# Kernel tuning notes

Hardware: AMD Instinct MI355X
Metric: run time of the kernel (lower is better)

Reference implementation:

```python
import jax, jax.numpy as jnp
import numpy as np

N_ITEMS = 100000
N_USERS = 16384
HIST = 50
TEXT_DIM = 256
GCN_DIM = 128
HIDDEN_DIM = 512
TOWER_DIM = 128


def _l2norm(x, eps=1e-12):
    # F.normalize(dim=1): x / max(||x||, eps)
    n = jnp.sqrt(jnp.sum(x * x, axis=1, keepdims=True))
    return x / jnp.maximum(n, eps)


def setup_inputs() -> dict:
    key = jax.random.key(0)
    ks = jax.random.split(key, 10)
    s1i = 1.0 / np.sqrt(TEXT_DIM + GCN_DIM)
    s2i = 1.0 / np.sqrt(HIDDEN_DIM)
    s1u = 1.0 / np.sqrt(GCN_DIM + TOWER_DIM)
    return {
        "item_text_emb": jax.random.normal(ks[0], (N_ITEMS, TEXT_DIM), jnp.float32),
        "gcn_item_emb": jax.random.normal(ks[1], (N_ITEMS, GCN_DIM), jnp.float32),
        "gcn_user_emb": jax.random.normal(ks[2], (N_USERS, GCN_DIM), jnp.float32),
        "hist_idx": jax.random.randint(ks[3], (N_USERS, HIST), 0, N_ITEMS),
        "W1i": jax.random.normal(ks[4], (TEXT_DIM + GCN_DIM, HIDDEN_DIM), jnp.float32) * s1i,
        "b1i": jnp.zeros((HIDDEN_DIM,), jnp.float32),
        "W2i": jax.random.normal(ks[5], (HIDDEN_DIM, TOWER_DIM), jnp.float32) * s2i,
        "b2i": jnp.zeros((TOWER_DIM,), jnp.float32),
        "W1u": jax.random.normal(ks[6], (GCN_DIM + TOWER_DIM, HIDDEN_DIM), jnp.float32) * s1u,
        "b1u": jnp.zeros((HIDDEN_DIM,), jnp.float32),
        "W2u": jax.random.normal(ks[7], (HIDDEN_DIM, TOWER_DIM), jnp.float32) * s2i,
        "b2u": jnp.zeros((TOWER_DIM,), jnp.float32),
    }


def reference(item_text_emb, gcn_item_emb, gcn_user_emb, hist_idx,
              W1i, b1i, W2i, b2i, W1u, b1u, W2u, b2u):
    # encode_items: MLP over concat(text, gcn) features, then L2 normalize
    item_feat = jnp.concatenate([item_text_emb, gcn_item_emb], axis=1)  # [N_items, text+gcn]
    h = jax.nn.relu(item_feat @ W1i + b1i)
    item_emb = _l2norm(h @ W2i + b2i)  # [N_items, TOWER_DIM]
    # encode_users: per-user gather of history item embeddings + mean pooling
    hist = jnp.mean(item_emb[hist_idx], axis=1)  # [N_users, TOWER_DIM]
    fused = jnp.concatenate([gcn_user_emb, hist], axis=1)
    hu = jax.nn.relu(fused @ W1u + b1u)
    user_emb = _l2norm(hu @ W2u + b2u)  # [N_users, TOWER_DIM]
    return user_emb
```

## Files before the change

### kernel.cpp

```cpp
#include <hip/hip_runtime.h>
#include <hip/hip_bf16.h>

#define HIST 50
#define N_ITEMS 100000
#define N_USERS 16384

typedef __bf16 bf8 __attribute__((ext_vector_type(8)));
typedef float  f4  __attribute__((ext_vector_type(4)));

__device__ __forceinline__ unsigned short f2bf(float x) {
    unsigned u = __builtin_bit_cast(unsigned, x);
    u += 0x7fffu + ((u >> 16) & 1u);
    return (unsigned short)(u >> 16);
}
__device__ __forceinline__ float bf2f(unsigned b) {
    unsigned u = b << 16;
    return __builtin_bit_cast(float, u);
}

__global__ void pack_weights(const float* __restrict__ W1i, const float* __restrict__ W2i,
                             const float* __restrict__ W1u, const float* __restrict__ W2u,
                             unsigned short* __restrict__ dstbase)
{
    int i = blockIdx.x * 256 + threadIdx.x;
    const float* W; unsigned short* dst; int N, KS, loc;
    if (i < 24576)      { W = W1i; dst = dstbase;          N = 512; KS = 12; loc = i; }
    else if (i < 32768) { W = W2i; dst = dstbase + 196608; N = 128; KS = 16; loc = i - 24576; }
    else if (i < 49152) { W = W1u; dst = dstbase + 262144; N = 512; KS = 8;  loc = i - 32768; }
    else                { W = W2u; dst = dstbase + 393216; N = 128; KS = 16; loc = i - 49152; }
    int l = loc & 63, fi = loc >> 6;
    int ks = fi % KS, nt = fi / KS;
    int q = l >> 4, c = l & 15;
    const float* src = W + (size_t)(ks * 32 + q * 8) * N + nt * 16 + c;
    unsigned o[4];
    #pragma unroll
    for (int k = 0; k < 4; ++k) {
        unsigned lo = f2bf(src[(2 * k) * N]);
        unsigned hi = f2bf(src[(2 * k + 1) * N]);
        o[k] = lo | (hi << 16);
    }
    uint4 v; v.x = o[0]; v.y = o[1]; v.z = o[2]; v.w = o[3];
    ((uint4*)dst)[(size_t)(nt * KS + ks) * 64 + l] = v;
}

template<int NR, int KS1, int ASTR, bool OUT_BF16>
__device__ __forceinline__ void tower_core(
    unsigned short* U, const float* b1s, const float* b2s, float* sumsq,
    const bf8* __restrict__ w1f, const bf8* __restrict__ w2f,
    void* __restrict__ outp, int row0, int tid)
{
    const int HSTR = 520;
    const int l = tid & 63, w = tid >> 6;
    const int q = l >> 4, c = l & 15;

    f4 acc1[NR][4];
    #pragma unroll
    for (int i = 0; i < NR; ++i)
        #pragma unroll
        for (int j = 0; j < 4; ++j) acc1[i][j] = (f4)0.0f;

    const unsigned short* ap = U + c * ASTR + q * 8;
    bf8 bcur[4], bnxt[4];
    #pragma unroll
    for (int nt = 0; nt < 4; ++nt)
        bcur[nt] = w1f[(size_t)((w * 4 + nt) * KS1 + 0) * 64 + l];
    #pragma unroll
    for (int ks = 0; ks < KS1; ++ks) {
        if (ks + 1 < KS1) {
            #pragma unroll
            for (int nt = 0; nt < 4; ++nt)
                bnxt[nt] = w1f[(size_t)((w * 4 + nt) * KS1 + ks + 1) * 64 + l];
        }
        bf8 a[NR];
        #pragma unroll
        for (int rt = 0; rt < NR; ++rt)
            a[rt] = *(const bf8*)(ap + rt * 16 * ASTR + ks * 32);
        #pragma unroll
        for (int rt = 0; rt < NR; ++rt)
            #pragma unroll
            for (int nt = 0; nt < 4; ++nt)
                acc1[rt][nt] = __builtin_amdgcn_mfma_f32_16x16x32_bf16(a[rt], bcur[nt], acc1[rt][nt], 0, 0, 0);
        #pragma unroll
        for (int nt = 0; nt < 4; ++nt) bcur[nt] = bnxt[nt];
    }
    __syncthreads();

    #pragma unroll
    for (int nt = 0; nt < 4; ++nt) {
        int col = w * 64 + nt * 16 + c;
        float bias = b1s[col];
        #pragma unroll
        for (int rt = 0; rt < NR; ++rt)
            #pragma unroll
            for (int reg = 0; reg < 4; ++reg) {
                float h = fmaxf(acc1[rt][nt][reg] + bias, 0.0f);
                U[(rt * 16 + q * 4 + reg) * HSTR + col] = f2bf(h);
            }
    }
    __syncthreads();

    constexpr int NR2 = NR / 2;
    const int rg = w >> 2, jj = w & 3;
    f4 acc2[NR2][2];
    #pragma unroll
    for (int i = 0; i < NR2; ++i) { acc2[i][0] = (f4)0.0f; acc2[i][1] = (f4)0.0f; }

    const unsigned short* hp = U + (size_t)(rg * NR2 * 16 + c) * HSTR + q * 8;
    bf8 ccur[2], cnxt[2];
    ccur[0] = w2f[(size_t)((jj * 2 + 0) * 16 + 0) * 64 + l];
    ccur[1] = w2f[(size_t)((jj * 2 + 1) * 16 + 0) * 64 + l];
    #pragma unroll
    for (int ks = 0; ks < 16; ++ks) {
        if (ks + 1 < 16) {
            cnxt[0] = w2f[(size_t)((jj * 2 + 0) * 16 + ks + 1) * 64 + l];
            cnxt[1] = w2f[(size_t)((jj * 2 + 1) * 16 + ks + 1) * 64 + l];
        }
        bf8 a[NR2];
        #pragma unroll
        for (int i = 0; i < NR2; ++i)
            a[i] = *(const bf8*)(hp + i * 16 * HSTR + ks * 32);
        #pragma unroll
        for (int i = 0; i < NR2; ++i) {
            acc2[i][0] = __builtin_amdgcn_mfma_f32_16x16x32_bf16(a[i], ccur[0], acc2[i][0], 0, 0, 0);
            acc2[i][1] = __builtin_amdgcn_mfma_f32_16x16x32_bf16(a[i], ccur[1], acc2[i][1], 0, 0, 0);
        }
        ccur[0] = cnxt[0]; ccur[1] = cnxt[1];
    }

    float v[NR2][2][4];
    #pragma unroll
    for (int i = 0; i < NR2; ++i)
        #pragma unroll
        for (int j = 0; j < 2; ++j) {
            float bias = b2s[jj * 32 + j * 16 + c];
            #pragma unroll
            for (int reg = 0; reg < 4; ++reg)
                v[i][j][reg] = acc2[i][j][reg] + bias;
        }
    #pragma unroll
    for (int i = 0; i < NR2; ++i)
        #pragma unroll
        for (int reg = 0; reg < 4; ++reg) {
            float s = v[i][0][reg] * v[i][0][reg] + v[i][1][reg] * v[i][1][reg];
            s += __shfl_xor(s, 1); s += __shfl_xor(s, 2);
            s += __shfl_xor(s, 4); s += __shfl_xor(s, 8);
            if (c == 0) atomicAdd(&sumsq[rg * NR2 * 16 + i * 16 + q * 4 + reg], s);
        }
    __syncthreads();
    #pragma unroll
    for (int i = 0; i < NR2; ++i)
        #pragma unroll
        for (int reg = 0; reg < 4; ++reg) {
            int row = rg * NR2 * 16 + i * 16 + q * 4 + reg;
            float inv = 1.0f / fmaxf(sqrtf(sumsq[row]), 1e-12f);
            #pragma unroll
            for (int j = 0; j < 2; ++j) {
                int col = jj * 32 + j * 16 + c;
                float o = v[i][j][reg] * inv;
                if (OUT_BF16)
                    ((unsigned short*)outp)[(size_t)(row0 + row) * 128 + col] = f2bf(o);
                else
                    ((float*)outp)[(size_t)(row0 + row) * 128 + col] = o;
            }
        }
}

#define ASI 392
#define ASU 264

__global__ __launch_bounds__(512, 4) void item_kernel(
    const float* __restrict__ text, const float* __restrict__ gcn,
    const bf8* __restrict__ w1f, const float* __restrict__ b1,
    const bf8* __restrict__ w2f, const float* __restrict__ b2,
    unsigned short* __restrict__ item_bf)
{
    __shared__ __align__(16) unsigned short U[32 * 520];
    __shared__ float b1s[512], b2s[128], sumsq[32];
    const int tid = threadIdx.x;
    const int row0 = blockIdx.x * 32;
    const float4* t4 = (const float4*)text;
    const float4* g4 = (const float4*)gcn;
    #pragma unroll
    for (int j = 0; j < 4; ++j) {
        int idx = tid + j * 512; int r = idx >> 6, c4 = idx & 63;
        float4 x = t4[(size_t)(row0 + r) * 64 + c4];
        ushort4 s; s.x = f2bf(x.x); s.y = f2bf(x.y); s.z = f2bf(x.z); s.w = f2bf(x.w);
        *(ushort4*)(U + r * ASI + c4 * 4) = s;
    }
    #pragma unroll
    for (int j = 0; j < 2; ++j) {
        int idx = tid + j * 512; int r = idx >> 5, c4 = idx & 31;
        float4 x = g4[(size_t)(row0 + r) * 32 + c4];
        ushort4 s; s.x = f2bf(x.x); s.y = f2bf(x.y); s.z = f2bf(x.z); s.w = f2bf(x.w);
        *(ushort4*)(U + r * ASI + 256 + c4 * 4) = s;
    }
    b1s[tid] = b1[tid];
    if (tid < 128) b2s[tid] = b2[tid];
    if (tid < 32)  sumsq[tid] = 0.0f;
    __syncthreads();
    tower_core<2, 12, ASI, true>(U, b1s, b2s, sumsq, w1f, w2f, item_bf, row0, tid);
}

__global__ __launch_bounds__(512, 4) void user_kernel(
    const float* __restrict__ gcnu, const int* __restrict__ hist,
    const unsigned short* __restrict__ item_bf,
    const bf8* __restrict__ w1f, const float* __restrict__ b1,
    const bf8* __restrict__ w2f, const float* __restrict__ b2,
    float* __restrict__ outp)
{
    __shared__ __align__(16) unsigned short U[32 * 520];
    __shared__ float b1s[512], b2s[128], sumsq[32];
    const int tid = threadIdx.x;
    const int u0 = blockIdx.x * 32;
    int* hist_s = (int*)(U + 32 * ASU);
    const float4* g4 = (const float4*)gcnu;
    #pragma unroll
    for (int j = 0; j < 2; ++j) {
        int idx = tid + j * 512; int r = idx >> 5, c4 = idx & 31;
        float4 x = g4[(size_t)(u0 + r) * 32 + c4];
        ushort4 s; s.x = f2bf(x.x); s.y = f2bf(x.y); s.z = f2bf(x.z); s.w = f2bf(x.w);
        *(ushort4*)(U + r * ASU + c4 * 4) = s;
    }
    for (int k = tid; k < 32 * HIST; k += 512)
        hist_s[k] = hist[(size_t)u0 * HIST + k];
    b1s[tid] = b1[tid];
    if (tid < 128) b2s[tid] = b2[tid];
    if (tid < 32)  sumsq[tid] = 0.0f;
    __syncthreads();
    {
        const int u = tid >> 4, g = tid & 15;
        int ids[HIST];
        #pragma unroll
        for (int t = 0; t < HIST; ++t) ids[t] = hist_s[u * HIST + t];
        float f[8];
        #pragma unroll
        for (int k = 0; k < 8; ++k) f[k] = 0.0f;
        #pragma unroll
        for (int t = 0; t < HIST; ++t) {
            uint4 x = *(const uint4*)(item_bf + (size_t)ids[t] * 128 + g * 8);
            unsigned vs[4] = {x.x, x.y, x.z, x.w};
            #pragma unroll
            for (int k = 0; k < 4; ++k) {
                f[2 * k]     += bf2f(vs[k] & 0xffffu);
                f[2 * k + 1] += bf2f(vs[k] >> 16);
            }
        }
        unsigned o[4];
        #pragma unroll
        for (int k = 0; k < 4; ++k)
            o[k] = (unsigned)f2bf(f[2 * k] * 0.02f) | ((unsigned)f2bf(f[2 * k + 1] * 0.02f) << 16);
        uint4 s; s.x = o[0]; s.y = o[1]; s.z = o[2]; s.w = o[3];
        *(uint4*)(U + u * ASU + 128 + g * 8) = s;
    }
    __syncthreads();
    tower_core<2, 8, ASU, false>(U, b1s, b2s, sumsq, w1f, w2f, outp, u0, tid);
}

extern "C" void kernel_launch(void* const* d_in, const int* in_sizes, int n_in,
                              void* d_out, int out_size, void* d_ws, size_t ws_size,
                              hipStream_t stream) {
    const float* text = (const float*)d_in[0];
    const float* gcni = (const float*)d_in[1];
    const float* gcnu = (const float*)d_in[2];
    const int*   hist = (const int*)d_in[3];
    const float* W1i  = (const float*)d_in[4];
    const float* b1i  = (const float*)d_in[5];
    const float* W2i  = (const float*)d_in[6];
    const float* b2i  = (const float*)d_in[7];
    const float* W1u  = (const float*)d_in[8];
    const float* b1u  = (const float*)d_in[9];
    const float* W2u  = (const float*)d_in[10];
    const float* b2u  = (const float*)d_in[11];
    float* out = (float*)d_out;

    unsigned short* itemb = (unsigned short*)d_ws;
    unsigned short* pw = itemb + 12800000;

    pack_weights<<<224, 256, 0, stream>>>(W1i, W2i, W1u, W2u, pw);
    item_kernel<<<N_ITEMS / 32, 512, 0, stream>>>(
        text, gcni, (const bf8*)pw, b1i, (const bf8*)(pw + 196608), b2i, itemb);
    user_kernel<<<N_USERS / 32, 512, 0, stream>>>(
        gcnu, hist, itemb, (const bf8*)(pw + 262144), b1u, (const bf8*)(pw + 393216), b2u, out);
}
```

Baseline: 305.7 us.

## Halve user-tower block rows and split history gather across two half-waves

The user kernel now processes 16 users per block instead of 32, doubling the grid to 1024 blocks and raising the occupancy hint to 8 blocks per CU. The history gather splits each user's 50 items across two 16-lane groups that are combined with a cross-lane shuffle, and tower_core gains an NR=1 specialization for its second GEMM stage. The aim is more parallelism and memory-level concurrency in the latency-bound gather across the 256 CUs. The cost is that each block reloads the user-tower weights for half as many rows, which doubles that weight traffic, and the MFMA tiles are less fully used.

```diff
diff --git a/kernel.cpp b/kernel.cpp
--- a/kernel.cpp
+++ b/kernel.cpp
@@ -99,70 +99,110 @@
     }
     __syncthreads();
 
-    constexpr int NR2 = NR / 2;
-    const int rg = w >> 2, jj = w & 3;
-    f4 acc2[NR2][2];
-    #pragma unroll
-    for (int i = 0; i < NR2; ++i) { acc2[i][0] = (f4)0.0f; acc2[i][1] = (f4)0.0f; }
-
-    const unsigned short* hp = U + (size_t)(rg * NR2 * 16 + c) * HSTR + q * 8;
-    bf8 ccur[2], cnxt[2];
-    ccur[0] = w2f[(size_t)((jj * 2 + 0) * 16 + 0) * 64 + l];
-    ccur[1] = w2f[(size_t)((jj * 2 + 1) * 16 + 0) * 64 + l];
-    #pragma unroll
-    for (int ks = 0; ks < 16; ++ks) {
-        if (ks + 1 < 16) {
-            cnxt[0] = w2f[(size_t)((jj * 2 + 0) * 16 + ks + 1) * 64 + l];
-            cnxt[1] = w2f[(size_t)((jj * 2 + 1) * 16 + ks + 1) * 64 + l];
-        }
-        bf8 a[NR2];
+    if constexpr (NR >= 2) {
+        constexpr int NR2 = NR / 2;
+        const int rg = w >> 2, jj = w & 3;
+        f4 acc2[NR2][2];
+        #pragma unroll
+        for (int i = 0; i < NR2; ++i) { acc2[i][0] = (f4)0.0f; acc2[i][1] = (f4)0.0f; }
+
+        const unsigned short* hp = U + (size_t)(rg * NR2 * 16 + c) * HSTR + q * 8;
+        bf8 ccur[2], cnxt[2];
+        ccur[0] = w2f[(size_t)((jj * 2 + 0) * 16 + 0) * 64 + l];
+        ccur[1] = w2f[(size_t)((jj * 2 + 1) * 16 + 0) * 64 + l];
+        #pragma unroll
+        for (int ks = 0; ks < 16; ++ks) {
+            if (ks + 1 < 16) {
+                cnxt[0] = w2f[(size_t)((jj * 2 + 0) * 16 + ks + 1) * 64 + l];
+                cnxt[1] = w2f[(size_t)((jj * 2 + 1) * 16 + ks + 1) * 64 + l];
+            }
+            bf8 a[NR2];
+            #pragma unroll
+            for (int i = 0; i < NR2; ++i)
+                a[i] = *(const bf8*)(hp + i * 16 * HSTR + ks * 32);
+            #pragma unroll
+            for (int i = 0; i < NR2; ++i) {
+                acc2[i][0] = __builtin_amdgcn_mfma_f32_16x16x32_bf16(a[i], ccur[0], acc2[i][0], 0, 0, 0);
+                acc2[i][1] = __builtin_amdgcn_mfma_f32_16x16x32_bf16(a[i], ccur[1], acc2[i][1], 0, 0, 0);
+            }
+            ccur[0] = cnxt[0]; ccur[1] = cnxt[1];
+        }
+
+        float v[NR2][2][4];
         #pragma unroll
         for (int i = 0; i < NR2; ++i)
-            a[i] = *(const bf8*)(hp + i * 16 * HSTR + ks * 32);
-        #pragma unroll
-        for (int i = 0; i < NR2; ++i) {
-            acc2[i][0] = __builtin_amdgcn_mfma_f32_16x16x32_bf16(a[i], ccur[0], acc2[i][0], 0, 0, 0);
-            acc2[i][1] = __builtin_amdgcn_mfma_f32_16x16x32_bf16(a[i], ccur[1], acc2[i][1], 0, 0, 0);
-        }
-        ccur[0] = cnxt[0]; ccur[1] = cnxt[1];
-    }
-
-    float v[NR2][2][4];
-    #pragma unroll
-    for (int i = 0; i < NR2; ++i)
-        #pragma unroll
-        for (int j = 0; j < 2; ++j) {
-            float bias = b2s[jj * 32 + j * 16 + c];
-            #pragma unroll
-            for (int reg = 0; reg < 4; ++reg)
-                v[i][j][reg] = acc2[i][j][reg] + bias;
-        }
-    #pragma unroll
-    for (int i = 0; i < NR2; ++i)
+            #pragma unroll
+            for (int j = 0; j < 2; ++j) {
+                float bias = b2s[jj * 32 + j * 16 + c];
+                #pragma unroll
+                for (int reg = 0; reg < 4; ++reg)
+                    v[i][j][reg] = acc2[i][j][reg] + bias;
+            }
+        #pragma unroll
+        for (int i = 0; i < NR2; ++i)
+            #pragma unroll
+            for (int reg = 0; reg < 4; ++reg) {
+                float s = v[i][0][reg] * v[i][0][reg] + v[i][1][reg] * v[i][1][reg];
+                s += __shfl_xor(s, 1); s += __shfl_xor(s, 2);
+                s += __shfl_xor(s, 4); s += __shfl_xor(s, 8);
+                if (c == 0) atomicAdd(&sumsq[rg * NR2 * 16 + i * 16 + q * 4 + reg], s);
+            }
+        __syncthreads();
+        #pragma unroll
+        for (int i = 0; i < NR2; ++i)
+            #pragma unroll
+            for (int reg = 0; reg < 4; ++reg) {
+                int row = rg * NR2 * 16 + i * 16 + q * 4 + reg;
+                float inv = 1.0f / fmaxf(sqrtf(sumsq[row]), 1e-12f);
+                #pragma unroll
+                for (int j = 0; j < 2; ++j) {
+                    int col = jj * 32 + j * 16 + c;
+                    float o = v[i][j][reg] * inv;
+                    if (OUT_BF16)
+                        ((unsigned short*)outp)[(size_t)(row0 + row) * 128 + col] = f2bf(o);
+                    else
+                        ((float*)outp)[(size_t)(row0 + row) * 128 + col] = o;
+                }
+            }
+    } else {
+        const int jj = w;
+        f4 acc2 = (f4)0.0f;
+        const unsigned short* hp = U + (size_t)c * HSTR + q * 8;
+        bf8 ccur = w2f[(size_t)(jj * 16 + 0) * 64 + l];
+        bf8 cnxt = ccur;
+        #pragma unroll
+        for (int ks = 0; ks < 16; ++ks) {
+            if (ks + 1 < 16)
+                cnxt = w2f[(size_t)(jj * 16 + ks + 1) * 64 + l];
+            bf8 a = *(const bf8*)(hp + ks * 32);
+            acc2 = __builtin_amdgcn_mfma_f32_16x16x32_bf16(a, ccur, acc2, 0, 0, 0);
+            ccur = cnxt;
+        }
+
+        float v[4];
+        float bias = b2s[jj * 16 + c];
+        #pragma unroll
+        for (int reg = 0; reg < 4; ++reg) v[reg] = acc2[reg] + bias;
         #pragma unroll
         for (int reg = 0; reg < 4; ++reg) {
-            float s = v[i][0][reg] * v[i][0][reg] + v[i][1][reg] * v[i][1][reg];
+            float s = v[reg] * v[reg];
             s += __shfl_xor(s, 1); s += __shfl_xor(s, 2);
             s += __shfl_xor(s, 4); s += __shfl_xor(s, 8);
-            if (c == 0) atomicAdd(&sumsq[rg * NR2 * 16 + i * 16 + q * 4 + reg], s);
-        }
-    __syncthreads();
-    #pragma unroll
-    for (int i = 0; i < NR2; ++i)
+            if (c == 0) atomicAdd(&sumsq[q * 4 + reg], s);
+        }
+        __syncthreads();
         #pragma unroll
         for (int reg = 0; reg < 4; ++reg) {
-            int row = rg * NR2 * 16 + i * 16 + q * 4 + reg;
+            int row = q * 4 + reg;
             float inv = 1.0f / fmaxf(sqrtf(sumsq[row]), 1e-12f);
-            #pragma unroll
-            for (int j = 0; j < 2; ++j) {
-                int col = jj * 32 + j * 16 + c;
-                float o = v[i][j][reg] * inv;
-                if (OUT_BF16)
-                    ((unsigned short*)outp)[(size_t)(row0 + row) * 128 + col] = f2bf(o);
-                else
-                    ((float*)outp)[(size_t)(row0 + row) * 128 + col] = o;
-            }
-        }
+            int col = jj * 16 + c;
+            float o = v[reg] * inv;
+            if (OUT_BF16)
+                ((unsigned short*)outp)[(size_t)(row0 + row) * 128 + col] = f2bf(o);
+            else
+                ((float*)outp)[(size_t)(row0 + row) * 128 + col] = o;
+        }
+    }
 }
 
 #define ASI 392
@@ -201,43 +241,41 @@
     tower_core<2, 12, ASI, true>(U, b1s, b2s, sumsq, w1f, w2f, item_bf, row0, tid);
 }
 
-__global__ __launch_bounds__(512, 4) void user_kernel(
+__global__ __launch_bounds__(512, 8) void user_kernel(
     const float* __restrict__ gcnu, const int* __restrict__ hist,
     const unsigned short* __restrict__ item_bf,
     const bf8* __restrict__ w1f, const float* __restrict__ b1,
     const bf8* __restrict__ w2f, const float* __restrict__ b2,
     float* __restrict__ outp)
 {
-    __shared__ __align__(16) unsigned short U[32 * 520];
-    __shared__ float b1s[512], b2s[128], sumsq[32];
+    __shared__ __align__(16) unsigned short U[16 * 520];
+    __shared__ float b1s[512], b2s[128], sumsq[16];
     const int tid = threadIdx.x;
-    const int u0 = blockIdx.x * 32;
-    int* hist_s = (int*)(U + 32 * ASU);
+    const int u0 = blockIdx.x * 16;
+    int* hist_s = (int*)(U + 16 * ASU);
     const float4* g4 = (const float4*)gcnu;
-    #pragma unroll
-    for (int j = 0; j < 2; ++j) {
-        int idx = tid + j * 512; int r = idx >> 5, c4 = idx & 31;
+    {
+        int r = tid >> 5, c4 = tid & 31;
         float4 x = g4[(size_t)(u0 + r) * 32 + c4];
         ushort4 s; s.x = f2bf(x.x); s.y = f2bf(x.y); s.z = f2bf(x.z); s.w = f2bf(x.w);
         *(ushort4*)(U + r * ASU + c4 * 4) = s;
     }
-    for (int k = tid; k < 32 * HIST; k += 512)
+    for (int k = tid; k < 16 * HIST; k += 512)
         hist_s[k] = hist[(size_t)u0 * HIST + k];
     b1s[tid] = b1[tid];
     if (tid < 128) b2s[tid] = b2[tid];
-    if (tid < 32)  sumsq[tid] = 0.0f;
+    if (tid < 16)  sumsq[tid] = 0.0f;
     __syncthreads();
     {
-        const int u = tid >> 4, g = tid & 15;
-        int ids[HIST];
-        #pragma unroll
-        for (int t = 0; t < HIST; ++t) ids[t] = hist_s[u * HIST + t];
+        const int u = tid >> 5, sub = tid & 31, h = sub >> 4, g = sub & 15;
         float f[8];
         #pragma unroll
         for (int k = 0; k < 8; ++k) f[k] = 0.0f;
-        #pragma unroll
-        for (int t = 0; t < HIST; ++t) {
-            uint4 x = *(const uint4*)(item_bf + (size_t)ids[t] * 128 + g * 8);
+        const int* hrow = hist_s + u * HIST + h * 25;
+        #pragma unroll
+        for (int t = 0; t < 25; ++t) {
+            int id = hrow[t];
+            uint4 x = *(const uint4*)(item_bf + (size_t)id * 128 + g * 8);
             unsigned vs[4] = {x.x, x.y, x.z, x.w};
             #pragma unroll
             for (int k = 0; k < 4; ++k) {
@@ -245,15 +283,19 @@
                 f[2 * k + 1] += bf2f(vs[k] >> 16);
             }
         }
-        unsigned o[4];
-        #pragma unroll
-        for (int k = 0; k < 4; ++k)
-            o[k] = (unsigned)f2bf(f[2 * k] * 0.02f) | ((unsigned)f2bf(f[2 * k + 1] * 0.02f) << 16);
-        uint4 s; s.x = o[0]; s.y = o[1]; s.z = o[2]; s.w = o[3];
-        *(uint4*)(U + u * ASU + 128 + g * 8) = s;
-    }
-    __syncthreads();
-    tower_core<2, 8, ASU, false>(U, b1s, b2s, sumsq, w1f, w2f, outp, u0, tid);
+        #pragma unroll
+        for (int k = 0; k < 8; ++k) f[k] += __shfl_xor(f[k], 16);
+        if (h == 0) {
+            unsigned o[4];
+            #pragma unroll
+            for (int k = 0; k < 4; ++k)
+                o[k] = (unsigned)f2bf(f[2 * k] * 0.02f) | ((unsigned)f2bf(f[2 * k + 1] * 0.02f) << 16);
+            uint4 s; s.x = o[0]; s.y = o[1]; s.z = o[2]; s.w = o[3];
+            *(uint4*)(U + u * ASU + 128 + g * 8) = s;
+        }
+    }
+    __syncthreads();
+    tower_core<1, 8, ASU, false>(U, b1s, b2s, sumsq, w1f, w2f, outp, u0, tid);
 }
 
 extern "C" void kernel_launch(void* const* d_in, const int* in_sizes, int n_in,
@@ -279,6 +321,6 @@
     pack_weights<<<224, 256, 0, stream>>>(W1i, W2i, W1u, W2u, pw);
     item_kernel<<<N_ITEMS / 32, 512, 0, stream>>>(
         text, gcni, (const bf8*)pw, b1i, (const bf8*)(pw + 196608), b2i, itemb);
-    user_kernel<<<N_USERS / 32, 512, 0, stream>>>(
+    user_kernel<<<N_USERS / 16, 512, 0, stream>>>(
         gcnu, hist, itemb, (const bf8*)(pw + 262144), b1u, (const bf8*)(pw + 393216), b2u, out);
 }
```

New measurement: 308.9 us. No clear change (+1.1%).

## Split history gather into separate high-occupancy kernel feeding user tower

Applied to the files above, without the earlier changes.

Moves the per-user history gather and mean pooling out of the user tower kernel into a dedicated gather kernel. That kernel uses small blocks, splits each user's 50 history items across two half-warps, and combines the halves with a shuffle. The pooled bf16 means go to a workspace buffer that the user kernel then loads directly, and the user kernel's launch bounds rise to 8 blocks per CU. The aim is more memory-level parallelism for the random gathers and lower register pressure in the tower kernel, at the cost of one extra launch and an extra write and read of a 16384x128 bf16 buffer.

```diff
diff --git a/kernel.cpp b/kernel.cpp
--- a/kernel.cpp
+++ b/kernel.cpp
@@ -201,9 +201,46 @@
     tower_core<2, 12, ASI, true>(U, b1s, b2s, sumsq, w1f, w2f, item_bf, row0, tid);
 }
 
-__global__ __launch_bounds__(512, 4) void user_kernel(
-    const float* __restrict__ gcnu, const int* __restrict__ hist,
-    const unsigned short* __restrict__ item_bf,
+__global__ __launch_bounds__(256, 8) void gather_kernel(
+    const int* __restrict__ hist, const unsigned short* __restrict__ item_bf,
+    unsigned short* __restrict__ hmean)
+{
+    __shared__ int ids[8 * HIST];
+    const int tid = threadIdx.x;
+    const int u0 = blockIdx.x * 8;
+    for (int k = tid; k < 8 * HIST; k += 256)
+        ids[k] = hist[(size_t)u0 * HIST + k];
+    __syncthreads();
+    const int u = tid >> 5, sub = tid & 31, h = sub >> 4, g = sub & 15;
+    float f[8];
+    #pragma unroll
+    for (int k = 0; k < 8; ++k) f[k] = 0.0f;
+    const int* hrow = ids + u * HIST + h * 25;
+    #pragma unroll
+    for (int t = 0; t < 25; ++t) {
+        int id = hrow[t];
+        uint4 x = *(const uint4*)(item_bf + (size_t)id * 128 + g * 8);
+        unsigned vs[4] = {x.x, x.y, x.z, x.w};
+        #pragma unroll
+        for (int k = 0; k < 4; ++k) {
+            f[2 * k]     += bf2f(vs[k] & 0xffffu);
+            f[2 * k + 1] += bf2f(vs[k] >> 16);
+        }
+    }
+    #pragma unroll
+    for (int k = 0; k < 8; ++k) f[k] += __shfl_xor(f[k], 16);
+    if (h == 0) {
+        unsigned o[4];
+        #pragma unroll
+        for (int k = 0; k < 4; ++k)
+            o[k] = (unsigned)f2bf(f[2 * k] * 0.02f) | ((unsigned)f2bf(f[2 * k + 1] * 0.02f) << 16);
+        uint4 s; s.x = o[0]; s.y = o[1]; s.z = o[2]; s.w = o[3];
+        *(uint4*)(hmean + (size_t)(u0 + u) * 128 + g * 8) = s;
+    }
+}
+
+__global__ __launch_bounds__(512, 8) void user_kernel(
+    const float* __restrict__ gcnu, const unsigned short* __restrict__ hmean,
     const bf8* __restrict__ w1f, const float* __restrict__ b1,
     const bf8* __restrict__ w2f, const float* __restrict__ b2,
     float* __restrict__ outp)
@@ -212,7 +249,6 @@
     __shared__ float b1s[512], b2s[128], sumsq[32];
     const int tid = threadIdx.x;
     const int u0 = blockIdx.x * 32;
-    int* hist_s = (int*)(U + 32 * ASU);
     const float4* g4 = (const float4*)gcnu;
     #pragma unroll
     for (int j = 0; j < 2; ++j) {
@@ -221,37 +257,14 @@
         ushort4 s; s.x = f2bf(x.x); s.y = f2bf(x.y); s.z = f2bf(x.z); s.w = f2bf(x.w);
         *(ushort4*)(U + r * ASU + c4 * 4) = s;
     }
-    for (int k = tid; k < 32 * HIST; k += 512)
-        hist_s[k] = hist[(size_t)u0 * HIST + k];
+    {
+        int r = tid >> 4, c8 = tid & 15;
+        uint4 x = *(const uint4*)(hmean + (size_t)(u0 + r) * 128 + c8 * 8);
+        *(uint4*)(U + r * ASU + 128 + c8 * 8) = x;
+    }
     b1s[tid] = b1[tid];
     if (tid < 128) b2s[tid] = b2[tid];
     if (tid < 32)  sumsq[tid] = 0.0f;
-    __syncthreads();
-    {
-        const int u = tid >> 4, g = tid & 15;
-        int ids[HIST];
-        #pragma unroll
-        for (int t = 0; t < HIST; ++t) ids[t] = hist_s[u * HIST + t];
-        float f[8];
-        #pragma unroll
-        for (int k = 0; k < 8; ++k) f[k] = 0.0f;
-        #pragma unroll
-        for (int t = 0; t < HIST; ++t) {
-            uint4 x = *(const uint4*)(item_bf + (size_t)ids[t] * 128 + g * 8);
-            unsigned vs[4] = {x.x, x.y, x.z, x.w};
-            #pragma unroll
-            for (int k = 0; k < 4; ++k) {
-                f[2 * k]     += bf2f(vs[k] & 0xffffu);
-                f[2 * k + 1] += bf2f(vs[k] >> 16);
-            }
-        }
-        unsigned o[4];
-        #pragma unroll
-        for (int k = 0; k < 4; ++k)
-            o[k] = (unsigned)f2bf(f[2 * k] * 0.02f) | ((unsigned)f2bf(f[2 * k + 1] * 0.02f) << 16);
-        uint4 s; s.x = o[0]; s.y = o[1]; s.z = o[2]; s.w = o[3];
-        *(uint4*)(U + u * ASU + 128 + g * 8) = s;
-    }
     __syncthreads();
     tower_core<2, 8, ASU, false>(U, b1s, b2s, sumsq, w1f, w2f, outp, u0, tid);
 }
@@ -274,11 +287,13 @@
     float* out = (float*)d_out;
 
     unsigned short* itemb = (unsigned short*)d_ws;
-    unsigned short* pw = itemb + 12800000;
+    unsigned short* pw    = itemb + 12800000;
+    unsigned short* hmean = pw + 458752;
 
     pack_weights<<<224, 256, 0, stream>>>(W1i, W2i, W1u, W2u, pw);
     item_kernel<<<N_ITEMS / 32, 512, 0, stream>>>(
         text, gcni, (const bf8*)pw, b1i, (const bf8*)(pw + 196608), b2i, itemb);
+    gather_kernel<<<N_USERS / 8, 256, 0, stream>>>(hist, itemb, hmean);
     user_kernel<<<N_USERS / 32, 512, 0, stream>>>(
-        gcnu, hist, itemb, (const bf8*)(pw + 262144), b1u, (const bf8*)(pw + 393216), b2u, out);
-}
+        gcnu, hmean, (const bf8*)(pw + 262144), b1u, (const bf8*)(pw + 393216), b2u, out);
+}
```

New measurement: 320.4 us. +4.8%, slower.
